# Kernel optimization log

Measured on AMD Instinct MI355X. Metric: run time of the kernel, lower is better.

## Reference

```python
import jax, jax.numpy as jnp
import numpy as np

EPS = 1e-5

def setup_inputs() -> dict:
    key = jax.random.key(0)
    k1, k2 = jax.random.split(key)
    x = jax.random.normal(k1, (32, 256, 56, 56), dtype=jnp.float32)
    # Conv2d(in=2, out=1, k=7, bias=False) weight: [out, in, kh, kw]
    conv_w = jax.random.normal(k2, (1, 2, 7, 7), dtype=jnp.float32) * 0.1
    # BatchNorm2d(1) params/buffers (eval mode)
    gamma = jnp.ones((1,), dtype=jnp.float32)
    beta = jnp.zeros((1,), dtype=jnp.float32)
    running_mean = jnp.zeros((1,), dtype=jnp.float32)
    running_var = jnp.ones((1,), dtype=jnp.float32)
    return {"x": x, "conv_w": conv_w, "gamma": gamma, "beta": beta,
            "running_mean": running_mean, "running_var": running_var}

def reference(x, conv_w, gamma, beta, running_mean, running_var):
    # channel-wise max & mean -> [B,2,H,W]
    max_result = jnp.max(x, axis=1, keepdims=True)
    avg_result = jnp.mean(x, axis=1, keepdims=True)
    result = jnp.concatenate([max_result, avg_result], axis=1)
    # 7x7 conv, pad=3, NCHW / OIHW
    out = jax.lax.conv_general_dilated(
        result, conv_w, window_strides=(1, 1), padding=((3, 3), (3, 3)),
        dimension_numbers=("NCHW", "OIHW", "NCHW"))
    # BatchNorm2d(1), eval mode with running stats
    inv = gamma / jnp.sqrt(running_var + EPS)
    out = (out - running_mean[None, :, None, None]) * inv[None, :, None, None] + beta[None, :, None, None]
    gate = jax.nn.sigmoid(out)  # [B,1,H,W]
    return x * gate
```

## Files before the change

kernel.cpp:

```cpp
#include <hip/hip_runtime.h>
#include <math.h>

#define NB 32
#define NC 256
#define SH 56
#define SW 56
#define HW 3136
#define HW4 784

__global__ __launch_bounds__(256) void k_reduce(const float4* __restrict__ x,
                                                float4* __restrict__ mx_out,
                                                float4* __restrict__ av_out) {
    __shared__ float4 smax[8][32];
    __shared__ float4 ssum[8][32];
    const int tid = threadIdx.x;
    const int pos = tid & 31;
    const int cg  = tid >> 5;
    const unsigned g = blockIdx.x * 32u + pos;
    const int b  = (int)(g / HW4);
    const int p4 = (int)(g - (unsigned)b * HW4);
    const float4* base = x + ((size_t)b * NC) * HW4 + p4 + (size_t)(cg * 32) * HW4;

    const float NEG = -__builtin_inff();
    float4 vmax = make_float4(NEG, NEG, NEG, NEG);
    float4 vsum = make_float4(0.f, 0.f, 0.f, 0.f);
    #pragma unroll 8
    for (int c = 0; c < 32; ++c) {
        float4 v = base[(size_t)c * HW4];
        vmax.x = fmaxf(vmax.x, v.x); vmax.y = fmaxf(vmax.y, v.y);
        vmax.z = fmaxf(vmax.z, v.z); vmax.w = fmaxf(vmax.w, v.w);
        vsum.x += v.x; vsum.y += v.y; vsum.z += v.z; vsum.w += v.w;
    }
    smax[cg][pos] = vmax;
    ssum[cg][pos] = vsum;
    __syncthreads();
    if (tid < 32) {
        float4 m = smax[0][tid];
        float4 s = ssum[0][tid];
        #pragma unroll
        for (int q = 1; q < 8; ++q) {
            float4 mm = smax[q][tid];
            float4 ss = ssum[q][tid];
            m.x = fmaxf(m.x, mm.x); m.y = fmaxf(m.y, mm.y);
            m.z = fmaxf(m.z, mm.z); m.w = fmaxf(m.w, mm.w);
            s.x += ss.x; s.y += ss.y; s.z += ss.z; s.w += ss.w;
        }
        const float r = 1.0f / 256.0f;
        s.x *= r; s.y *= r; s.z *= r; s.w *= r;
        const unsigned go = blockIdx.x * 32u + tid;
        mx_out[go] = m;
        av_out[go] = s;
    }
}

__global__ __launch_bounds__(256) void k_conv_mul(const float* __restrict__ mx,
                                                  const float* __restrict__ av,
                                                  const float* __restrict__ cw,
                                                  const float* __restrict__ gamma,
                                                  const float* __restrict__ beta,
                                                  const float* __restrict__ rmean,
                                                  const float* __restrict__ rvar,
                                                  const float4* __restrict__ x,
                                                  float4* __restrict__ out) {
    __shared__ float sw[98];
    __shared__ float sbias;
    __shared__ float4 sgate4[28];

    const int tid = threadIdx.x;
    const int b  = blockIdx.x / 28;
    const int rp = blockIdx.x - b * 28;

    const float inv = gamma[0] * rsqrtf(rvar[0] + 1e-5f);
    if (tid < 98) sw[tid] = cw[tid] * inv;
    if (tid == 0) sbias = beta[0] - rmean[0] * inv;
    __syncthreads();

    if (tid < 112) {
        const int h = rp * 2 + (tid / 56 ? 1 : 0) + 0 * tid;
        const int hr = rp * 2 + (tid >= 56 ? 1 : 0);
        const int w  = tid - (tid >= 56 ? 56 : 0);
        const float* mrow = mx + (size_t)b * HW;
        const float* arow = av + (size_t)b * HW;
        float acc = sbias;
        #pragma unroll
        for (int kh = 0; kh < 7; ++kh) {
            const int hh = hr + kh - 3;
            if (hh < 0 || hh >= SH) continue;
            #pragma unroll
            for (int kw = 0; kw < 7; ++kw) {
                const int ww = w + kw - 3;
                if (ww < 0 || ww >= SW) continue;
                const int q = hh * SW + ww;
                acc += mrow[q] * sw[kh * 7 + kw] + arow[q] * sw[49 + kh * 7 + kw];
            }
        }
        ((float*)sgate4)[tid] = 1.0f / (1.0f + expf(-acc));
        (void)h;
    }
    __syncthreads();

    const size_t strip = (size_t)b * NC * HW4 + (size_t)rp * 28;
    #pragma unroll 4
    for (int it = 0; it < 28; ++it) {
        const unsigned idx = (unsigned)it * 256u + (unsigned)tid;
        const unsigned c = idx / 28u;
        const unsigned q = idx - c * 28u;
        const size_t off = strip + (size_t)c * HW4 + q;
        const float4 g  = sgate4[q];
        const float4 xv = x[off];
        out[off] = make_float4(xv.x * g.x, xv.y * g.y, xv.z * g.z, xv.w * g.w);
    }
}

extern "C" void kernel_launch(void* const* d_in, const int* in_sizes, int n_in,
                              void* d_out, int out_size, void* d_ws, size_t ws_size,
                              hipStream_t stream) {
    const float* x     = (const float*)d_in[0];
    const float* cw    = (const float*)d_in[1];
    const float* gamma = (const float*)d_in[2];
    const float* beta  = (const float*)d_in[3];
    const float* rmean = (const float*)d_in[4];
    const float* rvar  = (const float*)d_in[5];
    float* out = (float*)d_out;

    float* mx_p = (float*)d_ws;
    float* av_p = mx_p + (size_t)NB * HW;

    k_reduce<<<(NB * HW4) / 32, 256, 0, stream>>>(
        (const float4*)x, (float4*)mx_p, (float4*)av_p);

    k_conv_mul<<<NB * 28, 256, 0, stream>>>(
        mx_p, av_p, cw, gamma, beta, rmean, rvar,
        (const float4*)x, (float4*)out);
}
```

Baseline: 63.10 us.

## Split channel reduction into per-group partials and finish reduction in gate kernel via LDS

The reduce kernel now has each block sweep a contiguous half-plane for a 32-channel group and write partial max/sum per group, with no shared-memory combine. The gate kernel folds the 8 partials for the rows it needs into shared-memory staging rows, then runs the 7x7 conv from LDS instead of global memory. The aim is more contiguous, coalesced reads in the reduce pass and cheaper conv loads. In exchange the partial workspace grows eightfold and each gate block re-reads overlapping halo rows of the partials.

```diff
diff --git a/kernel.cpp b/kernel.cpp
--- a/kernel.cpp
+++ b/kernel.cpp
@@ -7,54 +7,48 @@
 #define SW 56
 #define HW 3136
 #define HW4 784
+#define PERB4 (NC * HW4)
+#define NCG 8
 
-__global__ __launch_bounds__(256) void k_reduce(const float4* __restrict__ x,
-                                                float4* __restrict__ mx_out,
-                                                float4* __restrict__ av_out) {
-    __shared__ float4 smax[8][32];
-    __shared__ float4 ssum[8][32];
-    const int tid = threadIdx.x;
-    const int pos = tid & 31;
-    const int cg  = tid >> 5;
-    const unsigned g = blockIdx.x * 32u + pos;
-    const int b  = (int)(g / HW4);
-    const int p4 = (int)(g - (unsigned)b * HW4);
-    const float4* base = x + ((size_t)b * NC) * HW4 + p4 + (size_t)(cg * 32) * HW4;
+__device__ __forceinline__ float4 max4(float4 a, float4 b) {
+    return make_float4(fmaxf(a.x,b.x), fmaxf(a.y,b.y), fmaxf(a.z,b.z), fmaxf(a.w,b.w));
+}
+__device__ __forceinline__ float4 add4(float4 a, float4 b) {
+    return make_float4(a.x+b.x, a.y+b.y, a.z+b.z, a.w+b.w);
+}
+
+__global__ __launch_bounds__(256) void k_reduce_lin(const float4* __restrict__ x,
+                                                    float4* __restrict__ pmax,
+                                                    float4* __restrict__ psum) {
+    const int tid  = threadIdx.x;
+    const int bid  = blockIdx.x;
+    const int half = bid & 1;
+    const int bcg  = bid >> 1;
+    const float4* base = x + (size_t)bcg * (32 * HW4) + half * 392;
 
     const float NEG = -__builtin_inff();
-    float4 vmax = make_float4(NEG, NEG, NEG, NEG);
-    float4 vsum = make_float4(0.f, 0.f, 0.f, 0.f);
-    #pragma unroll 8
+    float4 m0 = make_float4(NEG,NEG,NEG,NEG), s0 = make_float4(0,0,0,0);
+    float4 m1 = m0, s1 = s0;
+    #pragma unroll 4
     for (int c = 0; c < 32; ++c) {
-        float4 v = base[(size_t)c * HW4];
-        vmax.x = fmaxf(vmax.x, v.x); vmax.y = fmaxf(vmax.y, v.y);
-        vmax.z = fmaxf(vmax.z, v.z); vmax.w = fmaxf(vmax.w, v.w);
-        vsum.x += v.x; vsum.y += v.y; vsum.z += v.z; vsum.w += v.w;
+        const float4 v0 = base[c * HW4 + tid];
+        m0 = max4(m0, v0); s0 = add4(s0, v0);
+        if (tid < 136) {
+            const float4 v1 = base[c * HW4 + 256 + tid];
+            m1 = max4(m1, v1); s1 = add4(s1, v1);
+        }
     }
-    smax[cg][pos] = vmax;
-    ssum[cg][pos] = vsum;
-    __syncthreads();
-    if (tid < 32) {
-        float4 m = smax[0][tid];
-        float4 s = ssum[0][tid];
-        #pragma unroll
-        for (int q = 1; q < 8; ++q) {
-            float4 mm = smax[q][tid];
-            float4 ss = ssum[q][tid];
-            m.x = fmaxf(m.x, mm.x); m.y = fmaxf(m.y, mm.y);
-            m.z = fmaxf(m.z, mm.z); m.w = fmaxf(m.w, mm.w);
-            s.x += ss.x; s.y += ss.y; s.z += ss.z; s.w += ss.w;
-        }
-        const float r = 1.0f / 256.0f;
-        s.x *= r; s.y *= r; s.z *= r; s.w *= r;
-        const unsigned go = blockIdx.x * 32u + tid;
-        mx_out[go] = m;
-        av_out[go] = s;
+    const size_t obase = (size_t)bcg * HW4 + half * 392;
+    pmax[obase + tid] = m0;
+    psum[obase + tid] = s0;
+    if (tid < 136) {
+        pmax[obase + 256 + tid] = m1;
+        psum[obase + 256 + tid] = s1;
     }
 }
 
-__global__ __launch_bounds__(256) void k_conv_mul(const float* __restrict__ mx,
-                                                  const float* __restrict__ av,
+__global__ __launch_bounds__(256) void k_gate_mul(const float4* __restrict__ pmax,
+                                                  const float4* __restrict__ psum,
                                                   const float* __restrict__ cw,
                                                   const float* __restrict__ gamma,
                                                   const float* __restrict__ beta,
@@ -62,8 +56,9 @@
                                                   const float* __restrict__ rvar,
                                                   const float4* __restrict__ x,
                                                   float4* __restrict__ out) {
-    __shared__ float sw[98];
-    __shared__ float sbias;
+    __shared__ float sw[99];
+    __shared__ __align__(16) float smx[8 * SW];
+    __shared__ __align__(16) float sav[8 * SW];
     __shared__ float4 sgate4[28];
 
     const int tid = threadIdx.x;
@@ -72,34 +67,55 @@
 
     const float inv = gamma[0] * rsqrtf(rvar[0] + 1e-5f);
     if (tid < 98) sw[tid] = cw[tid] * inv;
-    if (tid == 0) sbias = beta[0] - rmean[0] * inv;
+    if (tid == 0) sw[98] = beta[0] - rmean[0] * inv;
+
+    const int r0  = 2 * rp - 3;
+    const int rlo = r0 > 0 ? r0 : 0;
+    const int rhi = (2 * rp + 4) < (SH - 1) ? (2 * rp + 4) : (SH - 1);
+    const int n4  = (rhi - rlo + 1) * 14;
+    const int sh4 = (rlo - r0) * 14;
+
+    if (tid < n4) {
+        const size_t pb = (size_t)(b * NCG) * HW4 + rlo * 14 + tid;
+        float4 m = pmax[pb];
+        #pragma unroll
+        for (int cg = 1; cg < NCG; ++cg) m = max4(m, pmax[pb + (size_t)cg * HW4]);
+        ((float4*)smx)[sh4 + tid] = m;
+    } else if (tid >= 128 && tid - 128 < n4) {
+        const int t = tid - 128;
+        const size_t pb = (size_t)(b * NCG) * HW4 + rlo * 14 + t;
+        float4 s = psum[pb];
+        #pragma unroll
+        for (int cg = 1; cg < NCG; ++cg) s = add4(s, psum[pb + (size_t)cg * HW4]);
+        const float r = 1.0f / 256.0f;
+        s.x *= r; s.y *= r; s.z *= r; s.w *= r;
+        ((float4*)sav)[sh4 + t] = s;
+    }
     __syncthreads();
 
     if (tid < 112) {
-        const int h = rp * 2 + (tid / 56 ? 1 : 0) + 0 * tid;
-        const int hr = rp * 2 + (tid >= 56 ? 1 : 0);
-        const int w  = tid - (tid >= 56 ? 56 : 0);
-        const float* mrow = mx + (size_t)b * HW;
-        const float* arow = av + (size_t)b * HW;
-        float acc = sbias;
+        const int lr = tid >= 56 ? 1 : 0;
+        const int w  = tid - lr * 56;
+        const int hr = 2 * rp + lr;
+        float acc = sw[98];
         #pragma unroll
         for (int kh = 0; kh < 7; ++kh) {
             const int hh = hr + kh - 3;
             if (hh < 0 || hh >= SH) continue;
+            const int slot = lr + kh;
             #pragma unroll
             for (int kw = 0; kw < 7; ++kw) {
                 const int ww = w + kw - 3;
                 if (ww < 0 || ww >= SW) continue;
-                const int q = hh * SW + ww;
-                acc += mrow[q] * sw[kh * 7 + kw] + arow[q] * sw[49 + kh * 7 + kw];
+                acc += smx[slot * SW + ww] * sw[kh * 7 + kw]
+                     + sav[slot * SW + ww] * sw[49 + kh * 7 + kw];
             }
         }
         ((float*)sgate4)[tid] = 1.0f / (1.0f + expf(-acc));
-        (void)h;
     }
     __syncthreads();
 
-    const size_t strip = (size_t)b * NC * HW4 + (size_t)rp * 28;
+    const size_t strip = (size_t)b * PERB4 + (size_t)rp * 28;
     #pragma unroll 4
     for (int it = 0; it < 28; ++it) {
         const unsigned idx = (unsigned)it * 256u + (unsigned)tid;
@@ -123,13 +139,12 @@
     const float* rvar  = (const float*)d_in[5];
     float* out = (float*)d_out;
 
-    float* mx_p = (float*)d_ws;
-    float* av_p = mx_p + (size_t)NB * HW;
+    float4* pmax = (float4*)d_ws;
+    float4* psum = pmax + (size_t)NB * NCG * HW4;
 
-    k_reduce<<<(NB * HW4) / 32, 256, 0, stream>>>(
-        (const float4*)x, (float4*)mx_p, (float4*)av_p);
+    k_reduce_lin<<<NB * NCG * 2, 256, 0, stream>>>((const float4*)x, pmax, psum);
 
-    k_conv_mul<<<NB * 28, 256, 0, stream>>>(
-        mx_p, av_p, cw, gamma, beta, rmean, rvar,
+    k_gate_mul<<<NB * 28, 256, 0, stream>>>(
+        pmax, psum, cw, gamma, beta, rmean, rvar,
         (const float4*)x, (float4*)out);
 }
```

Result: no change. 63.85 us (+1.2%).
